# Optimization experiments

Measured on AMD Instinct MI355X. Metric: run time of the kernel, lower is better.

## Reference

```python
import jax, jax.numpy as jnp
import numpy as np

DIM = 256
HEADS = 8
SEQ = 4096
SCALE = DIM ** -0.5  # note: original scales by full dim, not head dim


def setup_inputs() -> dict:
    key = jax.random.key(0)
    ks = jax.random.split(key, 5)
    x = jax.random.normal(ks[0], (SEQ, DIM), dtype=jnp.float32)
    w_qkv = jax.random.normal(ks[1], (DIM, 3 * DIM), dtype=jnp.float32) * (DIM ** -0.5)
    b_qkv = jnp.zeros((3 * DIM,), dtype=jnp.float32)
    w_out = jax.random.normal(ks[2], (DIM, DIM), dtype=jnp.float32) * (DIM ** -0.5)
    b_out = jnp.zeros((DIM,), dtype=jnp.float32)
    return {"x": x, "w_qkv": w_qkv, "b_qkv": b_qkv, "w_out": w_out, "b_out": b_out}


def reference(x, w_qkv, b_qkv, w_out, b_out):
    n, dim = x.shape
    h = HEADS
    d = dim // h
    qkv = x @ w_qkv + b_qkv                      # [n, 3*dim]
    q, k, v = jnp.split(qkv, 3, axis=-1)         # each [n, dim]
    # 'n (h d) -> h n d'
    q = q.reshape(n, h, d).transpose(1, 0, 2)
    k = k.reshape(n, h, d).transpose(1, 0, 2)
    v = v.reshape(n, h, d).transpose(1, 0, 2)
    dots = jnp.einsum('hid,hjd->hij', q, k) * SCALE  # [h, n, n]
    attn = jax.nn.softmax(dots, axis=-1)
    out = jnp.einsum('hij,hjd->hid', attn, v)        # [h, n, d]
    out = out.transpose(1, 0, 2).reshape(n, dim)     # 'h n d -> n (h d)'
    return out @ w_out + b_out                       # [n, dim]
```

## Files before the change

kernel.cpp:

```cpp
#include <hip/hip_runtime.h>
#include <stdint.h>

#define SEQ   4096
#define DIM   256
#define HDIM  32
#define HEADS 8
#define W3    768
#define LOG2E 1.4426950408889634f

typedef float  f32x4  __attribute__((ext_vector_type(4)));
typedef short  bf16x8 __attribute__((ext_vector_type(8)));
typedef short  bf16x4 __attribute__((ext_vector_type(4)));

static __device__ __forceinline__ f32x4 MFMA_PV(bf16x4 a, bf16x4 b, f32x4 c) {
#if defined(__HIP_DEVICE_COMPILE__)
# if __has_builtin(__builtin_amdgcn_mfma_f32_16x16x16_bf16)
    return __builtin_amdgcn_mfma_f32_16x16x16_bf16(a, b, c, 0, 0, 0);
# elif __has_builtin(__builtin_amdgcn_mfma_f32_16x16x16bf16_1k)
    return __builtin_amdgcn_mfma_f32_16x16x16bf16_1k(a, b, c, 0, 0, 0);
# else
    f32x4 d;
    asm volatile("v_mfma_f32_16x16x16_bf16 %0, %1, %2, %3"
                 : "=v"(d) : "v"(a), "v"(b), "v"(c));
    return d;
# endif
#else
    (void)a; (void)b;
    return c;
#endif
}

__device__ __forceinline__ unsigned short f2bf(float f) {
    union { __bf16 h; unsigned short u; } v;
    v.h = (__bf16)f;
    return v.u;
}
__device__ __forceinline__ short f2bf_s(float f) {
    union { __bf16 h; short s; } v;
    v.h = (__bf16)f;
    return v.s;
}

__global__ __launch_bounds__(256) void prep_kernel(
    const float* __restrict__ x, const float* __restrict__ wqkv,
    const float* __restrict__ wout,
    unsigned short* __restrict__ xb,
    unsigned short* __restrict__ wt,
    unsigned short* __restrict__ wot)
{
    const int NX = SEQ * DIM;
    const int NW = DIM * W3;
    const int NO = DIM * DIM;
    const int total = NX + NW + NO;
    for (int i = blockIdx.x * blockDim.x + threadIdx.x; i < total;
         i += gridDim.x * blockDim.x) {
        if (i < NX) {
            xb[i] = f2bf(x[i]);
        } else if (i < NX + NW) {
            int j = i - NX;
            int col = j >> 8;
            int k   = j & 255;
            wt[j] = f2bf(wqkv[k * W3 + col]);
        } else {
            int j = i - NX - NW;
            int col = j >> 8;
            int k   = j & 255;
            wot[j] = f2bf(wout[k * DIM + col]);
        }
    }
}

__global__ __launch_bounds__(256) void qkv_gemm(
    const unsigned short* __restrict__ xb,
    const unsigned short* __restrict__ wt,
    const float* __restrict__ bqkv,
    unsigned short* __restrict__ Qb,
    unsigned short* __restrict__ Kb,
    unsigned short* __restrict__ Vb)
{
    const int wid  = threadIdx.x >> 6;
    const int lane = threadIdx.x & 63;
    const int g    = lane >> 4, li = lane & 15;
    const int row0 = blockIdx.x * 64 + wid * 16;
    const int col0 = blockIdx.y * 64;

    f32x4 acc[4];
    #pragma unroll
    for (int c = 0; c < 4; ++c)
        acc[c] = (f32x4){0.f, 0.f, 0.f, 0.f};

    #pragma unroll
    for (int ks = 0; ks < DIM; ks += 32) {
        bf16x8 a = *(const bf16x8*)(xb + (size_t)(row0 + li) * DIM + ks + g * 8);
        bf16x8 b[4];
        #pragma unroll
        for (int c = 0; c < 4; ++c)
            b[c] = *(const bf16x8*)(wt + (size_t)(col0 + 16 * c + li) * DIM + ks + g * 8);
        #pragma unroll
        for (int c = 0; c < 4; ++c)
            acc[c] = __builtin_amdgcn_mfma_f32_16x16x32_bf16(a, b[c], acc[c], 0, 0, 0);
    }

    #pragma unroll
    for (int c = 0; c < 4; ++c)
        #pragma unroll
        for (int r = 0; r < 4; ++r) {
            int row = row0 + g * 4 + r;
            int col = col0 + 16 * c + li;
            float v = acc[c][r] + bqkv[col];
            int sec = col >> 8;
            int cc  = col & 255;
            int hh  = cc >> 5, dd = cc & 31;
            if (sec == 0)
                Qb[((size_t)hh * SEQ + row) * HDIM + dd] = f2bf(v * (0.0625f * LOG2E));
            else if (sec == 1)
                Kb[((size_t)hh * SEQ + row) * HDIM + dd] = f2bf(v);
            else
                Vb[(size_t)hh * SEQ * HDIM + ((size_t)(row >> 4) * HDIM + dd) * 16 + (row & 15)] = f2bf(v);
        }
}

__global__ __launch_bounds__(256) void attn_kernel(
    const unsigned short* __restrict__ Qb,
    const unsigned short* __restrict__ Kb,
    const unsigned short* __restrict__ Vb,
    float* __restrict__ Opart,
    float* __restrict__ Lp,
    int nc)
{
    const int wid  = threadIdx.x >> 6;
    const int lane = threadIdx.x & 63;
    const int g    = lane >> 4, li = lane & 15;
    const int head = blockIdx.y;
    const int chunk = blockIdx.z;
    const int r0   = blockIdx.x * 128 + wid * 32;
    const int span = SEQ / nc;
    const int jb0 = chunk * span, jb1 = jb0 + span;

    const unsigned short* Qh = Qb + (size_t)head * SEQ * HDIM;
    const unsigned short* kbase = Kb + (size_t)head * SEQ * HDIM + (size_t)li * HDIM + g * 8;
    const unsigned short* vbase = Vb + (size_t)head * SEQ * HDIM + (size_t)li * 16 + 4 * g;

    bf16x8 aq[2];
    #pragma unroll
    for (int t = 0; t < 2; ++t)
        aq[t] = *(const bf16x8*)(Qh + (size_t)(r0 + 16 * t + li) * HDIM + g * 8);

    f32x4 o[2][2];
    #pragma unroll
    for (int t = 0; t < 2; ++t)
        #pragma unroll
        for (int nt = 0; nt < 2; ++nt)
            o[t][nt] = (f32x4){0.f, 0.f, 0.f, 0.f};
    float lacc[2] = {0.f, 0.f};

    const f32x4 zero4 = (f32x4){0.f, 0.f, 0.f, 0.f};

#define LOADK(DST, JB) do {                                                   \
    _Pragma("unroll")                                                         \
    for (int c_ = 0; c_ < 4; ++c_)                                            \
        DST[c_] = *(const bf16x8*)(kbase + (size_t)((JB) + 16 * c_) * HDIM);  \
} while (0)

#define TILE(BK, JB) do {                                                     \
    bf16x4 bv_[4][2];                                                         \
    _Pragma("unroll")                                                         \
    for (int c_ = 0; c_ < 4; ++c_)                                            \
        _Pragma("unroll")                                                     \
        for (int nt_ = 0; nt_ < 2; ++nt_)                                     \
            bv_[c_][nt_] = *(const bf16x4*)(vbase +                           \
                (size_t)(((JB) >> 4) + c_) * (HDIM * 16) + nt_ * 256);        \
    bf16x4 pa_[2][4];                                                         \
    _Pragma("unroll")                                                         \
    for (int t_ = 0; t_ < 2; ++t_) {                                          \
        f32x4 s_[4];                                                          \
        _Pragma("unroll")                                                     \
        for (int c_ = 0; c_ < 4; ++c_)                                        \
            s_[c_] = __builtin_amdgcn_mfma_f32_16x16x32_bf16(BK[c_], aq[t_], zero4, 0, 0, 0); \
        _Pragma("unroll")                                                     \
        for (int c_ = 0; c_ < 4; ++c_) {                                      \
            float p0_ = __builtin_amdgcn_exp2f(s_[c_][0]);                    \
            float p1_ = __builtin_amdgcn_exp2f(s_[c_][1]);                    \
            float p2_ = __builtin_amdgcn_exp2f(s_[c_][2]);                    \
            float p3_ = __builtin_amdgcn_exp2f(s_[c_][3]);                    \
            lacc[t_] += (p0_ + p1_) + (p2_ + p3_);                            \
            bf16x4 f_;                                                        \
            f_[0] = f2bf_s(p0_); f_[1] = f2bf_s(p1_);                         \
            f_[2] = f2bf_s(p2_); f_[3] = f2bf_s(p3_);                         \
            pa_[t_][c_] = f_;                                                 \
        }                                                                     \
    }                                                                         \
    _Pragma("unroll")                                                         \
    for (int c_ = 0; c_ < 4; ++c_)                                            \
        _Pragma("unroll")                                                     \
        for (int t_ = 0; t_ < 2; ++t_)                                        \
            _Pragma("unroll")                                                 \
            for (int nt_ = 0; nt_ < 2; ++nt_)                                 \
                o[t_][nt_] = MFMA_PV(pa_[t_][c_], bv_[c_][nt_], o[t_][nt_]);  \
} while (0)

    bf16x8 bkA[4], bkB[4];
    LOADK(bkA, jb0);
    for (int jb = jb0; jb < jb1; jb += 128) {
        LOADK(bkB, jb + 64);
        TILE(bkA, jb);
        int jbn = (jb + 128 < jb1) ? (jb + 128) : jb0;
        LOADK(bkA, jbn);
        TILE(bkB, jb + 64);
    }
#undef LOADK
#undef TILE

    #pragma unroll
    for (int t = 0; t < 2; ++t) {
        float L = lacc[t];
        L += __shfl_xor(L, 16);
        L += __shfl_xor(L, 32);
        lacc[t] = L;
    }

    float* Oc = Opart + (size_t)chunk * SEQ * DIM;
    #pragma unroll
    for (int t = 0; t < 2; ++t)
        #pragma unroll
        for (int nt = 0; nt < 2; ++nt)
            #pragma unroll
            for (int r = 0; r < 4; ++r) {
                int row = r0 + 16 * t + g * 4 + r;
                int col = head * HDIM + 16 * nt + li;
                Oc[(size_t)row * DIM + col] = o[t][nt][r];
            }
    if (lane < 16) {
        #pragma unroll
        for (int t = 0; t < 2; ++t) {
            int row = r0 + 16 * t + lane;
            Lp[((size_t)chunk * HEADS + head) * SEQ + row] = lacc[t];
        }
    }
}

__global__ __launch_bounds__(256) void combine_kernel(
    const float* __restrict__ Opart, const float* __restrict__ Lp,
    unsigned short* __restrict__ AO, int nc)
{
    int idx = blockIdx.x * 256 + threadIdx.x;
    int row = idx >> 7;
    int cp  = (idx & 127) << 1;
    int head = cp >> 5;
    float L = 0.f, a0 = 0.f, a1 = 0.f;
    for (int i = 0; i < nc; ++i) {
        L += Lp[((size_t)i * HEADS + head) * SEQ + row];
        const float* op = Opart + (size_t)i * SEQ * DIM + (size_t)row * DIM + cp;
        a0 += op[0];
        a1 += op[1];
    }
    float inv = 1.f / L;
    uint32_t pk = (uint32_t)f2bf(a0 * inv) | ((uint32_t)f2bf(a1 * inv) << 16);
    *reinterpret_cast<uint32_t*>(AO + (size_t)row * DIM + cp) = pk;
}

__global__ __launch_bounds__(256) void out_gemm(
    const unsigned short* __restrict__ AO,
    const unsigned short* __restrict__ wot,
    const float* __restrict__ bout,
    float* __restrict__ out)
{
    const int wid  = threadIdx.x >> 6;
    const int lane = threadIdx.x & 63;
    const int g    = lane >> 4, li = lane & 15;
    const int row0 = blockIdx.x * 64 + wid * 16;
    const int col0 = blockIdx.y * 64;

    f32x4 acc[4];
    #pragma unroll
    for (int c = 0; c < 4; ++c)
        acc[c] = (f32x4){0.f, 0.f, 0.f, 0.f};

    #pragma unroll
    for (int ks = 0; ks < DIM; ks += 32) {
        bf16x8 a = *(const bf16x8*)(AO + (size_t)(row0 + li) * DIM + ks + g * 8);
        bf16x8 b[4];
        #pragma unroll
        for (int c = 0; c < 4; ++c)
            b[c] = *(const bf16x8*)(wot + (size_t)(col0 + 16 * c + li) * DIM + ks + g * 8);
        #pragma unroll
        for (int c = 0; c < 4; ++c)
            acc[c] = __builtin_amdgcn_mfma_f32_16x16x32_bf16(a, b[c], acc[c], 0, 0, 0);
    }

    #pragma unroll
    for (int c = 0; c < 4; ++c)
        #pragma unroll
        for (int r = 0; r < 4; ++r) {
            int row = row0 + g * 4 + r;
            int col = col0 + 16 * c + li;
            out[(size_t)row * DIM + col] = acc[c][r] + bout[col];
        }
}

extern "C" void kernel_launch(void* const* d_in, const int* in_sizes, int n_in,
                              void* d_out, int out_size, void* d_ws, size_t ws_size,
                              hipStream_t stream)
{
    const float* x    = (const float*)d_in[0];
    const float* wqkv = (const float*)d_in[1];
    const float* bqkv = (const float*)d_in[2];
    const float* wout = (const float*)d_in[3];
    const float* bout = (const float*)d_in[4];
    float* out = (float*)d_out;

    char* ws = (char*)d_ws;
    const size_t OFF_XB  = 0;
    const size_t OFF_WT  = 2097152;
    const size_t OFF_WOT = 2490368;
    const size_t OFF_QB  = 2621440;
    const size_t OFF_KB  = 4718592;
    const size_t OFF_VT  = 6815744;
    const size_t OFF_AO  = 8912896;
    const size_t OFF_OP  = 11010048;
    const size_t OP_CH   = (size_t)SEQ * DIM * 4;
    const size_t LP_CH   = (size_t)HEADS * SEQ * 4;

    int nc = 8;
    while (nc > 1 && OFF_OP + (size_t)nc * (OP_CH + LP_CH) > ws_size) nc >>= 1;
    if (OFF_OP + (size_t)nc * (OP_CH + LP_CH) > ws_size) return;

    unsigned short* xb  = (unsigned short*)(ws + OFF_XB);
    unsigned short* wt  = (unsigned short*)(ws + OFF_WT);
    unsigned short* wot = (unsigned short*)(ws + OFF_WOT);
    unsigned short* Qb  = (unsigned short*)(ws + OFF_QB);
    unsigned short* Kb  = (unsigned short*)(ws + OFF_KB);
    unsigned short* Vb  = (unsigned short*)(ws + OFF_VT);
    unsigned short* AO  = (unsigned short*)(ws + OFF_AO);
    float* Opart = (float*)(ws + OFF_OP);
    float* Lp    = (float*)(ws + OFF_OP + (size_t)nc * OP_CH);

    hipLaunchKernelGGL(prep_kernel, dim3(2048), dim3(256), 0, stream,
                       x, wqkv, wout, xb, wt, wot);
    hipLaunchKernelGGL(qkv_gemm, dim3(64, 12), dim3(256), 0, stream,
                       xb, wt, bqkv, Qb, Kb, Vb);
    hipLaunchKernelGGL(attn_kernel, dim3(SEQ / 128, HEADS, nc), dim3(256), 0, stream,
                       Qb, Kb, Vb, Opart, Lp, nc);
    hipLaunchKernelGGL(combine_kernel, dim3(SEQ * DIM / 512), dim3(256), 0, stream,
                       Opart, Lp, AO, nc);
    hipLaunchKernelGGL(out_gemm, dim3(SEQ / 64, DIM / 64), dim3(256), 0, stream,
                       AO, wot, bout, out);
}
```

Measured before the change: 78.79 us.

## Tile-transpose weights in LDS, vectorize x cast, prefetch V and set MFMA priority

The prep kernel now transposes the weight matrices through a 64x65 shared-memory tile, so both reads and writes are coalesced instead of strided. It also casts x to bf16 with float4 loads, and the grid drops from 2048 blocks to 128. In the attention kernel, V fragments are double-buffered and loaded one tile ahead alongside K, using pointer increments instead of recomputed offsets. MFMA sections are wrapped in s_setprio to favour matrix issue across waves. The cost is higher register pressure from the extra V buffers, and the fixed loop bounds assume span/64 is even and at least 2.

```diff
diff --git a/kernel.cpp b/kernel.cpp
--- a/kernel.cpp
+++ b/kernel.cpp
@@ -9,6 +9,7 @@
 #define LOG2E 1.4426950408889634f
 
 typedef float  f32x4  __attribute__((ext_vector_type(4)));
+typedef float  fl4    __attribute__((ext_vector_type(4)));
 typedef short  bf16x8 __attribute__((ext_vector_type(8)));
 typedef short  bf16x4 __attribute__((ext_vector_type(4)));
 
@@ -48,24 +49,42 @@
     unsigned short* __restrict__ wt,
     unsigned short* __restrict__ wot)
 {
-    const int NX = SEQ * DIM;
-    const int NW = DIM * W3;
-    const int NO = DIM * DIM;
-    const int total = NX + NW + NO;
-    for (int i = blockIdx.x * blockDim.x + threadIdx.x; i < total;
-         i += gridDim.x * blockDim.x) {
-        if (i < NX) {
-            xb[i] = f2bf(x[i]);
-        } else if (i < NX + NW) {
-            int j = i - NX;
-            int col = j >> 8;
-            int k   = j & 255;
-            wt[j] = f2bf(wqkv[k * W3 + col]);
+    __shared__ float lds[64][65];
+    const int b   = blockIdx.x;
+    const int tid = threadIdx.x;
+    if (b < 64) {
+        const float* src;
+        unsigned short* dst;
+        int N, i0, j0;
+        if (b < 48) {
+            src = wqkv; dst = wt; N = W3;
+            i0 = (b & 3) * 64; j0 = (b >> 2) * 64;
         } else {
-            int j = i - NX - NW;
-            int col = j >> 8;
-            int k   = j & 255;
-            wot[j] = f2bf(wout[k * DIM + col]);
+            int bb = b - 48;
+            src = wout; dst = wot; N = DIM;
+            i0 = (bb & 3) * 64; j0 = (bb >> 2) * 64;
+        }
+        const int c = tid & 63, grp = tid >> 6;
+        #pragma unroll
+        for (int k = 0; k < 16; ++k) {
+            int r = grp * 16 + k;
+            lds[r][c] = src[(size_t)(i0 + r) * N + j0 + c];
+        }
+        __syncthreads();
+        #pragma unroll
+        for (int k = 0; k < 16; ++k) {
+            int cc = grp * 16 + k;
+            dst[(size_t)(j0 + cc) * DIM + i0 + c] = f2bf(lds[c][cc]);
+        }
+    } else {
+        const fl4* __restrict__ x4 = (const fl4*)x;
+        const int total4 = SEQ * DIM / 4;
+        for (int i = (b - 64) * 256 + tid; i < total4; i += 64 * 256) {
+            fl4 v = x4[i];
+            ushort4 o;
+            o.x = f2bf(v[0]); o.y = f2bf(v[1]);
+            o.z = f2bf(v[2]); o.w = f2bf(v[3]);
+            *reinterpret_cast<ushort4*>(xb + (size_t)i * 4) = o;
         }
     }
 }
@@ -135,11 +154,14 @@
     const int chunk = blockIdx.z;
     const int r0   = blockIdx.x * 128 + wid * 32;
     const int span = SEQ / nc;
-    const int jb0 = chunk * span, jb1 = jb0 + span;
+    const int jb0  = chunk * span;
+    const int ntile = span / 64;
 
     const unsigned short* Qh = Qb + (size_t)head * SEQ * HDIM;
-    const unsigned short* kbase = Kb + (size_t)head * SEQ * HDIM + (size_t)li * HDIM + g * 8;
-    const unsigned short* vbase = Vb + (size_t)head * SEQ * HDIM + (size_t)li * 16 + 4 * g;
+    const unsigned short* kp = Kb + (size_t)head * SEQ * HDIM + (size_t)jb0 * HDIM
+                             + (size_t)li * HDIM + g * 8;
+    const unsigned short* vp = Vb + (size_t)head * SEQ * HDIM + (size_t)jb0 * HDIM
+                             + (size_t)li * 16 + 4 * g;
 
     bf16x8 aq[2];
     #pragma unroll
@@ -156,27 +178,30 @@
 
     const f32x4 zero4 = (f32x4){0.f, 0.f, 0.f, 0.f};
 
-#define LOADK(DST, JB) do {                                                   \
+#define LOADK(DST, P) do {                                                    \
     _Pragma("unroll")                                                         \
     for (int c_ = 0; c_ < 4; ++c_)                                            \
-        DST[c_] = *(const bf16x8*)(kbase + (size_t)((JB) + 16 * c_) * HDIM);  \
+        DST[c_] = *(const bf16x8*)((P) + c_ * (16 * HDIM));                   \
 } while (0)
 
-#define TILE(BK, JB) do {                                                     \
-    bf16x4 bv_[4][2];                                                         \
+#define LOADV(DST, P) do {                                                    \
     _Pragma("unroll")                                                         \
     for (int c_ = 0; c_ < 4; ++c_)                                            \
         _Pragma("unroll")                                                     \
         for (int nt_ = 0; nt_ < 2; ++nt_)                                     \
-            bv_[c_][nt_] = *(const bf16x4*)(vbase +                           \
-                (size_t)(((JB) >> 4) + c_) * (HDIM * 16) + nt_ * 256);        \
+            DST[c_][nt_] = *(const bf16x4*)((P) + c_ * (16 * HDIM) + nt_ * 256); \
+} while (0)
+
+#define TILE(BK, BV) do {                                                     \
     bf16x4 pa_[2][4];                                                         \
     _Pragma("unroll")                                                         \
     for (int t_ = 0; t_ < 2; ++t_) {                                          \
         f32x4 s_[4];                                                          \
+        __builtin_amdgcn_s_setprio(1);                                        \
         _Pragma("unroll")                                                     \
         for (int c_ = 0; c_ < 4; ++c_)                                        \
             s_[c_] = __builtin_amdgcn_mfma_f32_16x16x32_bf16(BK[c_], aq[t_], zero4, 0, 0, 0); \
+        __builtin_amdgcn_s_setprio(0);                                        \
         _Pragma("unroll")                                                     \
         for (int c_ = 0; c_ < 4; ++c_) {                                      \
             float p0_ = __builtin_amdgcn_exp2f(s_[c_][0]);                    \
@@ -190,25 +215,36 @@
             pa_[t_][c_] = f_;                                                 \
         }                                                                     \
     }                                                                         \
+    __builtin_amdgcn_s_setprio(1);                                            \
     _Pragma("unroll")                                                         \
     for (int c_ = 0; c_ < 4; ++c_)                                            \
         _Pragma("unroll")                                                     \
         for (int t_ = 0; t_ < 2; ++t_)                                        \
             _Pragma("unroll")                                                 \
             for (int nt_ = 0; nt_ < 2; ++nt_)                                 \
-                o[t_][nt_] = MFMA_PV(pa_[t_][c_], bv_[c_][nt_], o[t_][nt_]);  \
+                o[t_][nt_] = MFMA_PV(pa_[t_][c_], BV[c_][nt_], o[t_][nt_]);   \
+    __builtin_amdgcn_s_setprio(0);                                            \
 } while (0)
 
     bf16x8 bkA[4], bkB[4];
-    LOADK(bkA, jb0);
-    for (int jb = jb0; jb < jb1; jb += 128) {
-        LOADK(bkB, jb + 64);
-        TILE(bkA, jb);
-        int jbn = (jb + 128 < jb1) ? (jb + 128) : jb0;
-        LOADK(bkA, jbn);
-        TILE(bkB, jb + 64);
-    }
+    bf16x4 bvA[4][2], bvB[4][2];
+    LOADK(bkA, kp);
+    LOADV(bvA, vp);
+    for (int i = 0; i < ntile - 2; i += 2) {
+        LOADK(bkB, kp + 2048);
+        LOADV(bvB, vp + 2048);
+        TILE(bkA, bvA);
+        LOADK(bkA, kp + 4096);
+        LOADV(bvA, vp + 4096);
+        TILE(bkB, bvB);
+        kp += 4096; vp += 4096;
+    }
+    LOADK(bkB, kp + 2048);
+    LOADV(bvB, vp + 2048);
+    TILE(bkA, bvA);
+    TILE(bkB, bvB);
 #undef LOADK
+#undef LOADV
 #undef TILE
 
     #pragma unroll
@@ -335,7 +371,7 @@
     float* Opart = (float*)(ws + OFF_OP);
     float* Lp    = (float*)(ws + OFF_OP + (size_t)nc * OP_CH);
 
-    hipLaunchKernelGGL(prep_kernel, dim3(2048), dim3(256), 0, stream,
+    hipLaunchKernelGGL(prep_kernel, dim3(128), dim3(256), 0, stream,
                        x, wqkv, wout, xb, wt, wot);
     hipLaunchKernelGGL(qkv_gemm, dim3(64, 12), dim3(256), 0, stream,
                        xb, wt, bqkv, Qb, Kb, Vb);
```

New measurement: 80.08 us. Within noise of the previous version (+1.6%).
